# Kernel tuning notes

Hardware: AMD Instinct MI355X
Metric: run time of the kernel (lower is better)

The kernel has to match this reference:

```python
import jax, jax.numpy as jnp
import numpy as np

B, IN_C, OUT_C, H, W = 16, 64, 64, 128, 128
MIN_R, MAX_R, BASE, SCALE = 1, 6, 3, 3


def setup_inputs() -> dict:
    key = jax.random.key(0)
    k1, k2 = jax.random.split(key)
    x = jax.random.normal(k1, (B, IN_C, H, W), dtype=jnp.float32)
    # kaiming-uniform-ish scale for a 3x3 conv weight
    weight = jax.random.normal(k2, (OUT_C, IN_C, 3, 3), dtype=jnp.float32) * (1.0 / np.sqrt(IN_C * 9))
    # truncated-normal-style integer dilation per output channel (deterministic)
    rng = np.random.default_rng(0)
    offsets = np.clip(np.round(rng.normal(BASE, SCALE, size=OUT_C)), MIN_R, MAX_R).astype(np.int32)
    return {"x": x, "weight": weight, "offsets": offsets}


def _gsd_conv(x, weight, offs_np):
    # Per-channel dilation conv: group channels by dilation, conv each group
    # (dilation=o, padding=o keeps HxW), scatter back to original channel order.
    out = jnp.zeros((x.shape[0], weight.shape[0], x.shape[2], x.shape[3]), dtype=x.dtype)
    for o in np.unique(offs_np):
        idx = np.nonzero(offs_np == o)[0]          # static channel indices for this dilation
        w = weight[idx]                             # [g, in_c, 3, 3]
        o = int(o)
        y = jax.lax.conv_general_dilated(
            x, w,
            window_strides=(1, 1),
            padding=[(o, o), (o, o)],
            rhs_dilation=(o, o),
            dimension_numbers=("NCHW", "OIHW", "NCHW"),
        )                                           # [B, g, H, W]
        out = out.at[:, idx].set(y)
    return out


def reference(x, weight, offsets):
    offs_np = np.asarray(offsets)
    return _gsd_conv(x, weight, offs_np)
```

## Files before the change

kernel.cpp:

```cpp
#include <hip/hip_runtime.h>


#define HW_ 128
#define C_ 64
#define B_ 16
#define EX 44
#define EY 28
#define NPIX (EY * EX)
#define NSETS 39
#define BUFDW (NSETS * 64 * 4)
#define PADW 140
#define PLANE_STRIDE (PADW * PADW * 16)
#define MAX_ITEMS 12
#define WS_WPACK_OFF 1024
#define WS_XB16_OFF (1 << 20)
#define XB16_BYTES ((size_t)B_ * 4 * PLANE_STRIDE * 2)


typedef __attribute__((ext_vector_type(8))) short short8;
typedef __attribute__((ext_vector_type(16))) float floatx16;

__device__ __forceinline__ unsigned bf16rne(float f) {
  unsigned u = __float_as_uint(f);
  return (u + 0x7FFFu + ((u >> 16) & 1u)) >> 16;
}

#define GLOAD_LDS16(g, l)                                   \
  __builtin_amdgcn_global_load_lds(                         \
      (const __attribute__((address_space(1))) void*)(g),   \
      (__attribute__((address_space(3))) void*)(l), 16, 0, 0)

__global__ __launch_bounds__(256) void gsd_prep(
    const float* __restrict__ x, const int* __restrict__ offsets,
    const float* __restrict__ w, int* __restrict__ desc,
    uint4* __restrict__ wpack, unsigned short* __restrict__ xb16,
    const int nrow) {
  const int bid = blockIdx.x;
  const int tid = threadIdx.x;

  if (bid < nrow) {
    const int b = bid / PADW, py = bid - b * PADW;
    uint4* o4 = (uint4*)xb16;
    const size_t pb0 = ((size_t)b * 4) * 39200 + (size_t)py * 280;
    const uint4 z = make_uint4(0, 0, 0, 0);
    if (py < 6 || py >= PADW - 6) {
      for (int i = tid; i < 1120; i += 256) {
        const int ks = i / 280, r = i - ks * 280;
        o4[pb0 + (size_t)ks * 39200 + r] = z;
      }
      return;
    }
    if (tid < 96) {
      const int ks = tid / 24, rr = tid - ks * 24;
      const int idx = rr < 12 ? rr : 256 + rr;
      o4[pb0 + (size_t)ks * 39200 + idx] = z;
    }
    const int y = py - 6;
    __shared__ unsigned l32[128 * 33];
    const int xx = tid & 127, ph = tid >> 7;
    const float* xp = x + (size_t)b * (C_ * HW_ * HW_) + y * HW_ + xx;
#pragma unroll 4
    for (int p = ph; p < 32; p += 2) {
      const float v0 = xp[(2 * p) * (HW_ * HW_)];
      const float v1 = xp[(2 * p + 1) * (HW_ * HW_)];
      l32[xx * 33 + p] = bf16rne(v0) | (bf16rne(v1) << 16);
    }
    __syncthreads();
#pragma unroll 4
    for (int ch = tid; ch < 1024; ch += 256) {
      const int ks = ch >> 8, r = ch & 255;
      const unsigned* s = &l32[(r >> 1) * 33 + ks * 8 + (r & 1) * 4];
      o4[pb0 + (size_t)ks * 39200 + 12 + r] = make_uint4(s[0], s[1], s[2], s[3]);
    }
    return;
  }

  __shared__ int sd[128];
  __shared__ int soffs[C_];
  if (tid < C_) soffs[tid] = offsets[tid];
  __syncthreads();
  if (tid < C_) {
    const int key = soffs[tid];
    int rank = 0;
    for (int c = 0; c < C_; ++c) {
      const int kc = soffs[c];
      rank += (int)((kc < key) | ((kc == key) & (c < tid)));
    }
    sd[rank] = tid;
  }
  __syncthreads();
  if (tid == 0) {
    int ni = 0, c = 0;
    while (c < C_ && ni < MAX_ITEMS) {
      const int d = soffs[sd[c]];
      int e = c;
      while (e < C_ && soffs[sd[e]] == d) ++e;
      for (int st = c; st < e && ni < MAX_ITEMS; st += 32) {
        sd[66 + ni] = d;
        sd[78 + ni] = st;
        sd[90 + ni] = (e - st) < 32 ? (e - st) : 32;
        ++ni;
      }
      c = e;
    }
    sd[64] = ni;
  }
  __syncthreads();

  const int sbid = bid - nrow;
  if (sbid == 0) {
    if (tid < 102) desc[tid] = sd[tid];
    return;
  }
  const int wix = sbid - 1;
  if (wix >= sd[64]) return;
  const int start = sd[78 + wix];
  const int g = sd[90 + wix];

  for (int i = tid; i < 4 * 9 * 64; i += 256) {
    const int ks = i / 576;
    const int r = i % 576;
    const int tap = r >> 6;
    const int lane = r & 63;
    const int m = lane & 31, hh = lane >> 5;
    const bool act = m < g;
    const int oc = act ? sd[start + m] : 0;
    unsigned ww[4];
    for (int jj = 0; jj < 4; ++jj) {
      float v0 = 0.f, v1 = 0.f;
      if (act) {
        const int ic0 = ks * 16 + hh * 8 + jj * 2;
        v0 = w[(oc * C_ + ic0) * 9 + tap];
        v1 = w[(oc * C_ + ic0 + 1) * 9 + tap];
      }
      ww[jj] = bf16rne(v0) | (bf16rne(v1) << 16);
    }
    wpack[(size_t)wix * 2304 + i] = make_uint4(ww[0], ww[1], ww[2], ww[3]);
  }
}

template <bool PRE>
__global__ __launch_bounds__(512, 2) void gsd_conv(
    const float* __restrict__ x, const unsigned short* __restrict__ xb16,
    const int* __restrict__ desc, const uint4* __restrict__ wpack,
    float* __restrict__ out) {
  const int tid = threadIdx.x;
  const int bid0 = blockIdx.x;
  const int gxid = (bid0 & 7) * 64 + (bid0 >> 3);
  const int b = gxid >> 5;
  const int yt = (gxid >> 2) & 7;
  const int xt = gxid & 3;
  const int y0 = yt * 16, x0 = xt * 32;

  const int lane = tid & 63;
  const int n = lane & 31;
  const int h = lane >> 5;
  const int wv = tid >> 6;
  const int yb = wv * 2;

  __shared__ __align__(16) unsigned ldsbuf[4 * BUFDW];

  if constexpr (PRE) {
    const unsigned short* xbase = xb16 + (size_t)b * 4 * PLANE_STRIDE;
    int srcoff[5];
#pragma unroll
    for (int j = 0; j < 5; ++j) {
      const int q = (wv + j * 8) * 64 + lane;
      int pix = q >> 1;
      if (pix > NPIX - 1) pix = NPIX - 1;
      const int p = q & 1;
      const int yy = pix / EX, xx = pix - yy * EX;
      const int half = p ^ ((pix >> 2) & 1);
      srcoff[j] = ((y0 + yy) * PADW + (x0 + xx)) * 16 + half * 8;
    }
#pragma unroll
    for (int ks = 0; ks < 4; ++ks) {
      const unsigned short* xp = xbase + (size_t)ks * PLANE_STRIDE;
#pragma unroll
      for (int j = 0; j < 5; ++j) {
        if (j < 4) {
          GLOAD_LDS16(xp + srcoff[j],
                      &ldsbuf[ks * BUFDW + (wv + j * 8) * 256]);
        } else if (wv < 7) {
          GLOAD_LDS16(xp + srcoff[4], &ldsbuf[ks * BUFDW + (wv + 32) * 256]);
        }
      }
    }
  } else {
    const int slx = tid & 63;
    const int sq = (tid >> 6) & 3;
    const int sy2 = tid >> 8;
    const float* xb = x + (size_t)b * (C_ * HW_ * HW_);
    const int gx = x0 - 6 + slx;
    const int gxc = gx < 0 ? 0 : (gx > 127 ? 127 : gx);
    const bool xin = ((unsigned)gx < 128u) & (slx < EX);
    for (int ks = 0; ks < 4; ++ks) {
      const float* xp = xb + (size_t)(ks * 16 + sq * 4) * (HW_ * HW_);
#pragma unroll 2
      for (int yy = sy2; yy < EY; yy += 2) {
        const int gy = y0 - 6 + yy;
        const int gyc = gy < 0 ? 0 : (gy > 127 ? 127 : gy);
        const bool ok = xin & ((unsigned)gy < 128u);
        const float* p = xp + gyc * HW_ + gxc;
        float v0 = p[0];
        float v1 = p[HW_ * HW_];
        float v2 = p[2 * HW_ * HW_];
        float v3 = p[3 * HW_ * HW_];
        if (!ok) { v0 = v1 = v2 = v3 = 0.f; }
        const unsigned lo = bf16rne(v0) | (bf16rne(v1) << 16);
        const unsigned hi = bf16rne(v2) | (bf16rne(v3) << 16);
        if (slx < EX) {
          const int pix = yy * EX + slx;
          const int dws = ks * BUFDW + pix * 8 +
                          (((sq >> 1) ^ ((pix >> 2) & 1)) << 2) +
                          ((sq & 1) << 1);
          *reinterpret_cast<uint2*>(&ldsbuf[dws]) = make_uint2(lo, hi);
        }
      }
    }
  }
  __syncthreads();

  const int cnt = __builtin_amdgcn_readfirstlane(desc[64]);

  for (int s = 0; s < cnt; ++s) {
    const int d = __builtin_amdgcn_readfirstlane(desc[66 + s]);
    const int start = __builtin_amdgcn_readfirstlane(desc[78 + s]);
    const int g = __builtin_amdgcn_readfirstlane(desc[90 + s]);

    floatx16 acc0, acc1;
#pragma unroll
    for (int e = 0; e < 16; ++e) { acc0[e] = 0.f; acc1[e] = 0.f; }

#pragma unroll
    for (int ks = 0; ks < 4; ++ks) {
      const uint4* wp = wpack + ((size_t)s * 4 + ks) * 576 + lane;
      const unsigned* cbuf = &ldsbuf[ks * BUFDW];
#pragma unroll
      for (int tap = 0; tap < 9; ++tap) {
        const int ky = tap / 3 - 1, kx = tap % 3 - 1;
        const short8 af = __builtin_bit_cast(short8, wp[tap * 64]);
        const int prow = yb + ky * d + 6;
        const int pxb = n + kx * d + 6;
        const int pix0 = prow * EX + pxb;
        const int pix1 = pix0 + EX;
        const int dws0 = (pix0 << 3) + ((h ^ ((pix0 >> 2) & 1)) << 2);
        const int dws1 = (pix1 << 3) + ((h ^ ((pix1 >> 2) & 1)) << 2);
        const short8 bf0 = *reinterpret_cast<const short8*>(&cbuf[dws0]);
        const short8 bf1 = *reinterpret_cast<const short8*>(&cbuf[dws1]);
        acc0 = __builtin_amdgcn_mfma_f32_32x32x16_bf16(af, bf0, acc0, 0, 0, 0);
        acc1 = __builtin_amdgcn_mfma_f32_32x32x16_bf16(af, bf1, acc1, 0, 0, 0);
      }
    }

#pragma unroll
    for (int reg = 0; reg < 16; ++reg) {
      const int row = (reg & 3) + 8 * (reg >> 2) + 4 * h;
      if (row < g) {
        const int oc = desc[start + row];
        float* op =
            &out[((size_t)(b * C_ + oc) * HW_ + (y0 + yb)) * HW_ + x0 + n];
        op[0] = acc0[reg];
        op[HW_] = acc1[reg];
      }
    }
  }
}

extern "C" void kernel_launch(void* const* d_in, const int* in_sizes, int n_in,
                              void* d_out, int out_size, void* d_ws,
                              size_t ws_size, hipStream_t stream) {
  const float* x = (const float*)d_in[0];
  const float* w = (const float*)d_in[1];
  const int* offsets = (const int*)d_in[2];
  float* out = (float*)d_out;

  int* desc = (int*)d_ws;
  uint4* wpack = (uint4*)((char*)d_ws + WS_WPACK_OFF);
  unsigned short* xb16 = (unsigned short*)((char*)d_ws + WS_XB16_OFF);

  const bool pre = ws_size >= (size_t)WS_XB16_OFF + XB16_BYTES;
  const int nrow = pre ? B_ * PADW : 0;

  gsd_prep<<<dim3(nrow + 1 + MAX_ITEMS), 256, 0, stream>>>(
      x, offsets, w, desc, wpack, xb16, nrow);
  if (pre) {
    gsd_conv<true><<<dim3(B_ * 8 * 4), 512, 0, stream>>>(
        x, xb16, desc, wpack, out);
  } else {
    gsd_conv<false><<<dim3(B_ * 8 * 4), 512, 0, stream>>>(
        x, xb16, desc, wpack, out);
  }
}
```

Measured before the change: 204.0 us.

## Split LDS input into separate channel-half planes and preload all weights per set

The interleaved, XOR-swizzled LDS layout of the bf16 input tile is replaced by two contiguous half-planes per k-slice, one for each 8-channel half, so each lane's B-fragment address becomes a simple linear offset. Both the prefetch path and the fallback conversion path write into the new layout. All 36 weight fragments for a dilation set are now loaded into registers before the MFMA loop instead of one load per tap. This is meant to cut address arithmetic and expose weight-load latency, at the cost of many more VGPRs (possible spills or lower occupancy under 512x2 launch bounds) and possibly more LDS bank conflicts without the swizzle.

```diff
diff --git a/kernel.cpp b/kernel.cpp
--- a/kernel.cpp
+++ b/kernel.cpp
@@ -8,7 +8,8 @@
 #define EY 28
 #define NPIX (EY * EX)
 #define NSETS 39
-#define BUFDW (NSETS * 64 * 4)
+#define HALFDW (NPIX * 4)
+#define PLANEDW (NSETS * 64 * 4)
 #define PADW 140
 #define PLANE_STRIDE (PADW * PADW * 16)
 #define MAX_ITEMS 12
@@ -158,31 +159,28 @@
   const int wv = tid >> 6;
   const int yb = wv * 2;
 
-  __shared__ __align__(16) unsigned ldsbuf[4 * BUFDW];
+  __shared__ __align__(16) unsigned ldsbuf[4 * PLANEDW];
 
   if constexpr (PRE) {
     const unsigned short* xbase = xb16 + (size_t)b * 4 * PLANE_STRIDE;
     int srcoff[5];
 #pragma unroll
     for (int j = 0; j < 5; ++j) {
-      const int q = (wv + j * 8) * 64 + lane;
-      int pix = q >> 1;
-      if (pix > NPIX - 1) pix = NPIX - 1;
-      const int p = q & 1;
+      int q = (wv + j * 8) * 64 + lane;
+      if (q > 2 * NPIX - 1) q = 2 * NPIX - 1;
+      const int p = q >= NPIX ? 1 : 0;
+      const int pix = q - p * NPIX;
       const int yy = pix / EX, xx = pix - yy * EX;
-      const int half = p ^ ((pix >> 2) & 1);
-      srcoff[j] = ((y0 + yy) * PADW + (x0 + xx)) * 16 + half * 8;
+      srcoff[j] = ((y0 + yy) * PADW + (x0 + xx)) * 16 + p * 8;
     }
 #pragma unroll
     for (int ks = 0; ks < 4; ++ks) {
       const unsigned short* xp = xbase + (size_t)ks * PLANE_STRIDE;
 #pragma unroll
       for (int j = 0; j < 5; ++j) {
-        if (j < 4) {
+        if (j < 4 || wv < 7) {
           GLOAD_LDS16(xp + srcoff[j],
-                      &ldsbuf[ks * BUFDW + (wv + j * 8) * 256]);
-        } else if (wv < 7) {
-          GLOAD_LDS16(xp + srcoff[4], &ldsbuf[ks * BUFDW + (wv + 32) * 256]);
+                      &ldsbuf[ks * PLANEDW + (wv + j * 8) * 256]);
         }
       }
     }
@@ -211,8 +209,7 @@
         const unsigned hi = bf16rne(v2) | (bf16rne(v3) << 16);
         if (slx < EX) {
           const int pix = yy * EX + slx;
-          const int dws = ks * BUFDW + pix * 8 +
-                          (((sq >> 1) ^ ((pix >> 2) & 1)) << 2) +
+          const int dws = ks * PLANEDW + (sq >> 1) * HALFDW + pix * 4 +
                           ((sq & 1) << 1);
           *reinterpret_cast<uint2*>(&ldsbuf[dws]) = make_uint2(lo, hi);
         }
@@ -222,35 +219,36 @@
   __syncthreads();
 
   const int cnt = __builtin_amdgcn_readfirstlane(desc[64]);
+  const int hbase = h * HALFDW;
 
   for (int s = 0; s < cnt; ++s) {
     const int d = __builtin_amdgcn_readfirstlane(desc[66 + s]);
     const int start = __builtin_amdgcn_readfirstlane(desc[78 + s]);
     const int g = __builtin_amdgcn_readfirstlane(desc[90 + s]);
 
+    const uint4* wp = wpack + (size_t)s * 2304 + lane;
+    uint4 af[36];
+#pragma unroll
+    for (int i = 0; i < 36; ++i) af[i] = wp[i * 64];
+
     floatx16 acc0, acc1;
 #pragma unroll
     for (int e = 0; e < 16; ++e) { acc0[e] = 0.f; acc1[e] = 0.f; }
 
 #pragma unroll
-    for (int ks = 0; ks < 4; ++ks) {
-      const uint4* wp = wpack + ((size_t)s * 4 + ks) * 576 + lane;
-      const unsigned* cbuf = &ldsbuf[ks * BUFDW];
-#pragma unroll
-      for (int tap = 0; tap < 9; ++tap) {
-        const int ky = tap / 3 - 1, kx = tap % 3 - 1;
-        const short8 af = __builtin_bit_cast(short8, wp[tap * 64]);
-        const int prow = yb + ky * d + 6;
-        const int pxb = n + kx * d + 6;
-        const int pix0 = prow * EX + pxb;
-        const int pix1 = pix0 + EX;
-        const int dws0 = (pix0 << 3) + ((h ^ ((pix0 >> 2) & 1)) << 2);
-        const int dws1 = (pix1 << 3) + ((h ^ ((pix1 >> 2) & 1)) << 2);
-        const short8 bf0 = *reinterpret_cast<const short8*>(&cbuf[dws0]);
-        const short8 bf1 = *reinterpret_cast<const short8*>(&cbuf[dws1]);
-        acc0 = __builtin_amdgcn_mfma_f32_32x32x16_bf16(af, bf0, acc0, 0, 0, 0);
-        acc1 = __builtin_amdgcn_mfma_f32_32x32x16_bf16(af, bf1, acc1, 0, 0, 0);
-      }
+    for (int i = 0; i < 36; ++i) {
+      const int ks = i / 9, tap = i % 9;
+      const int ky = tap / 3 - 1, kx = tap % 3 - 1;
+      const int prow = yb + ky * d + 6;
+      const int pxb = n + kx * d + 6;
+      const int pix0 = prow * EX + pxb;
+      const int pix1 = pix0 + EX;
+      const unsigned* cb = &ldsbuf[ks * PLANEDW + hbase];
+      const short8 bf0 = *reinterpret_cast<const short8*>(&cb[pix0 * 4]);
+      const short8 bf1 = *reinterpret_cast<const short8*>(&cb[pix1 * 4]);
+      const short8 a8 = __builtin_bit_cast(short8, af[i]);
+      acc0 = __builtin_amdgcn_mfma_f32_32x32x16_bf16(a8, bf0, acc0, 0, 0, 0);
+      acc1 = __builtin_amdgcn_mfma_f32_32x32x16_bf16(a8, bf1, acc1, 0, 0, 0);
     }
 
 #pragma unroll
```

New measurement: 211.3 us. 3.6% more time.
